# Kernel optimization log

Hardware: AMD Instinct MI355X
Metric: run time of the kernel (lower is better)

The kernel has to match this reference:

```python
import jax, jax.numpy as jnp
import numpy as np

N = 1536          # num nodes
E = 49152         # num edges (avg degree 32)
D_IN = 32         # in_channels_node
D_EA = 2          # in_channels_edge_attr
D_ET = 2          # in_channels_edge_type
EMB = 32          # edge_attr_emb = edge_type_emb = node_emb = out_channels
HEADS = 3
SLOPE = 0.2


def leaky(x):
    return jax.nn.leaky_relu(x, negative_slope=SLOPE)


def setup_inputs() -> dict:
    key = jax.random.key(0)
    ks = jax.random.split(key, 12)
    node_f = jax.random.normal(ks[0], (N, D_IN), dtype=jnp.float32)
    edge_index = jax.random.randint(ks[1], (2, E), 0, N, dtype=jnp.int32)
    edge_attr = jax.random.normal(ks[2], (E, D_EA), dtype=jnp.float32)
    edge_type = jax.random.uniform(ks[3], (E, D_ET), dtype=jnp.float32)
    veh_node_mask = jax.random.bernoulli(ks[4], 0.7, (N,))
    ped_node_mask = jnp.logical_not(veh_node_mask)
    s = 0.1
    W_veh = jax.random.normal(ks[5], (EMB, D_IN), dtype=jnp.float32) * s
    W_ped = jax.random.normal(ks[6], (EMB, D_IN), dtype=jnp.float32) * s
    W_ea = jax.random.normal(ks[7], (EMB, D_EA), dtype=jnp.float32) * s
    W_et = jax.random.normal(ks[8], (EMB, D_ET), dtype=jnp.float32) * s
    # attention_nn: Linear(edge_attr_emb + edge_type_emb + 2*node_emb -> heads)
    W_att = jax.random.normal(ks[9], (HEADS, 2 * EMB + 2 * EMB), dtype=jnp.float32) * s
    # node_update_emb: Linear(edge_attr_emb + node_emb -> out_channels)
    W_upd = jax.random.normal(ks[10], (EMB, 2 * EMB), dtype=jnp.float32) * s
    return dict(node_f=node_f, edge_attr=edge_attr, edge_type=edge_type,
                W_veh=W_veh, W_ped=W_ped, W_ea=W_ea, W_et=W_et,
                W_att=W_att, W_upd=W_upd,
                edge_index=edge_index, veh_node_mask=veh_node_mask,
                ped_node_mask=ped_node_mask)


def reference(node_f, edge_attr, edge_type, W_veh, W_ped, W_ea, W_et,
              W_att, W_upd, edge_index, veh_node_mask, ped_node_mask):
    n = node_f.shape[0]
    src, dst = edge_index[0], edge_index[1]

    # edge embeddings [E, 32] each
    emb_ea = leaky(edge_attr @ W_ea.T)
    emb_et = leaky(edge_type.astype(node_f.dtype) @ W_et.T)
    edge_f = jnp.concatenate([emb_ea, emb_et], axis=-1)        # [E, 64]

    # densify (sparse_coo_tensor -> to_dense sums duplicate indices)
    dense_edge = jnp.zeros((n, n, 2 * EMB), node_f.dtype).at[src, dst].add(edge_f)
    dense_ea = jnp.zeros((n, n, EMB), node_f.dtype).at[src, dst].add(emb_ea)
    adj = jnp.zeros((n, n), node_f.dtype).at[src, dst].add(1.0)

    # type-specific node embedding (ped assignment last, matching torch overwrite order)
    node_emb = jnp.where(veh_node_mask[:, None], node_f @ W_veh.T, 0.0)
    node_emb = jnp.where(ped_node_mask[:, None], node_f @ W_ped.T, node_emb)
    node_emb = leaky(node_emb)                                  # [N, 32]

    # attention scores: split the linear over the concatenated [tar | edge | nbr] features
    W_tar, W_edge, W_nbr = W_att[:, :EMB], W_att[:, EMB:3 * EMB], W_att[:, 3 * EMB:]
    scores = leaky((node_emb @ W_tar.T)[:, None, :]
                   + jnp.einsum('ijc,hc->ijh', dense_edge, W_edge)
                   + (node_emb @ W_nbr.T)[None, :, :])          # [N, N, H]

    scores = jnp.where(adj[:, :, None] == 0.0, jnp.float32(-10000.0), scores)
    attn = jax.nn.softmax(scores, axis=1)                       # softmax over neighbors

    # node update features: Linear over [edge_attr_emb | nbr_emb]; identical across heads
    Wu_e, Wu_n = W_upd[:, :EMB], W_upd[:, EMB:]
    upd = leaky(jnp.einsum('ijc,oc->ijo', dense_ea, Wu_e)
                + (node_emb @ Wu_n.T)[None, :, :])              # [N, N, 32]

    # weighted aggregation over neighbors, then concat heads
    next_node_f = jnp.einsum('ijh,ijo->iho', attn, upd)         # [N, H, 32]
    return next_node_f.reshape(n, HEADS * EMB)
```

## Files before the change

### kernel.cpp

```cpp
#include <hip/hip_runtime.h>
#include <stdint.h>

#define NN 1536
#define EE 49152
#define EMB 32
#define HEADS 3
#define SLOPE 0.2f
#define CAP 72
#define SES 67
#define EBLK (EE/256)
#define NBLK (NN/8)

__device__ __forceinline__ float lrelu(float x){ return x >= 0.f ? x : SLOPE*x; }

__device__ int detect_mask_layout(const unsigned char* p){
  const int* pi = (const int*)p;
  bool ok = true;
  for (int k=0;k<64 && ok;k++){ int v = pi[k]; ok = (v==0 || v==1); }
  if (ok) return 0;
  ok = true;
  for (int k=0;k<256 && ok;k++){ ok = (p[k] <= 1); }
  if (ok) return 1;
  return 2;
}
__device__ bool mask_at(const unsigned char* p, int layout, int i){
  if (layout==0) return ((const int*)p)[i] != 0;
  if (layout==1) return p[i] != 0;
  return ((const float*)p)[i] != 0.f;
}

__global__ __launch_bounds__(256) void k_prep(
    const float* __restrict__ node_f,
    const float* __restrict__ edge_attr, const float* __restrict__ edge_type,
    const float* __restrict__ W_veh, const float* __restrict__ W_ped,
    const float* __restrict__ W_att, const float* __restrict__ W_upd,
    const int* __restrict__ ei, const unsigned char* __restrict__ veh_mask,
    int* __restrict__ cnt, int* __restrict__ bucketD, float4* __restrict__ bucketF,
    float* __restrict__ tar, float* __restrict__ nbr, float* __restrict__ nb)
{
  const int t = threadIdx.x;
  const int b = blockIdx.x;

  if (b < EBLK){
    const int e = b*256 + t;
    const int s = ei[e], d = ei[EE + e];
    const float2 ea = ((const float2*)edge_attr)[e];
    const float2 et = ((const float2*)edge_type)[e];
    const int idx = atomicAdd(&cnt[s], 1);
    if (idx < CAP){
      bucketD[(size_t)s*CAP + idx] = d;
      bucketF[(size_t)s*CAP + idx] = make_float4(ea.x, ea.y, et.x, et.y);
    }
    return;
  }

  __shared__ float sWvehT[EMB*33], sWpedT[EMB*33], sWunT[EMB*33];
  __shared__ float sWt[HEADS*EMB], sWn[HEADS*EMB];
  __shared__ float sF[8*EMB], sEmb[8*EMB];
  __shared__ int layout_s;
  const int i0 = (b - EBLK)*8;
  if (t == 0) layout_s = detect_mask_layout(veh_mask);
  for (int idx=t; idx<EMB*EMB; idx+=256){
    const int mm = idx>>5, kk = idx&31;
    sWvehT[mm*33+kk] = W_veh[idx];
    sWpedT[mm*33+kk] = W_ped[idx];
    sWunT[mm*33+kk]  = W_upd[mm*64 + EMB + kk];
  }
  if (t < HEADS*EMB){
    const int h = t>>5, c = t&31;
    sWt[t] = W_att[h*128 + c];
    sWn[t] = W_att[h*128 + 96 + c];
  }
  sF[t] = node_f[(size_t)i0*EMB + t];
  __syncthreads();

  const int li = t >> 5, m = t & 31;
  const int i = i0 + li;
  const bool veh = mask_at(veh_mask, layout_s, i);
  const float* WT = veh ? sWvehT : sWpedT;
  float a = 0.f;
  #pragma unroll
  for (int k=0;k<EMB;k++) a += sF[li*EMB+k] * WT[m*33+k];
  sEmb[li*EMB+m] = lrelu(a);
  __syncthreads();

  float bb = 0.f;
  #pragma unroll
  for (int k=0;k<EMB;k++) bb += sEmb[li*EMB+k] * sWunT[m*33+k];
  nb[(size_t)i*EMB + m] = bb;
  if (m < 3){
    float v = 0.f;
    #pragma unroll
    for (int k=0;k<EMB;k++) v += sEmb[li*EMB+k] * sWt[m*EMB+k];
    tar[i*4+m] = v;
  } else if (m < 6){
    const int h = m-3;
    float v = 0.f;
    #pragma unroll
    for (int k=0;k<EMB;k++) v += sEmb[li*EMB+k] * sWn[h*EMB+k];
    nbr[i*4+h] = v;
  }
}

__global__ __launch_bounds__(256, 6) void k_rows(
    const int* __restrict__ cnt, const int* __restrict__ bucketD,
    const float4* __restrict__ bucketF,
    const float* __restrict__ W_ea, const float* __restrict__ W_et,
    const float* __restrict__ W_att, const float* __restrict__ W_upd,
    const float* __restrict__ tar, const float* __restrict__ nbr,
    const float* __restrict__ nb, float* __restrict__ out)
{
  const int r = blockIdx.x;
  const int t = threadIdx.x;

  __shared__ int   ld[CAP], canon[CAP], slotidx[CAP], slotof[CAP], cdst[CAP];
  __shared__ float4 pay[CAP];
  __shared__ float sE[CAP*SES];
  __shared__ float sWea[64], sWet[64], sWedge[HEADS*64];
  __shared__ float pp[HEADS*CAP];
  __shared__ float partial[4*96];
  __shared__ float hden[HEADS];
  __shared__ int np_s, hasdup_s;

  if (t < 64){ sWea[t] = W_ea[t]; sWet[t] = W_et[t]; }
  if (t < HEADS*64) sWedge[t] = W_att[(t>>6)*128 + EMB + (t&63)];
  if (t == 0){ np_s = 0; hasdup_s = 0; }

  const int K = min(cnt[r], CAP);

  if (K == 0){
    float* fb = pp;
    if (t < EMB) fb[t] = 0.f;
    __syncthreads();
    for (int idx=t; idx<NN*EMB; idx+=256) atomicAdd(&fb[idx&31], lrelu(nb[idx]));
    __syncthreads();
    if (t < 96) out[(size_t)r*96 + t] = fb[t&31] * (1.0f/NN);
    return;
  }

  for (int i=t; i<K; i+=256){
    const int d = bucketD[(size_t)r*CAP + i];
    ld[i]  = d;
    cdst[i] = d;
    pay[i] = bucketF[(size_t)r*CAP + i];
    canon[i] = i;
  }
  __syncthreads();

  for (int p=t; p<K*K; p+=256){
    const int i = p / K, j = p - i*K;
    if (j < i && ld[i] == ld[j]){ atomicMin(&canon[i], j); hasdup_s = 1; }
  }
  __syncthreads();

  const bool dup = (hasdup_s != 0);
  int Kc = K;
  if (dup){
    for (int i=t; i<K; i+=256){
      if (canon[i] == i){
        const int s2 = atomicAdd(&np_s, 1);
        slotidx[i] = s2;
        cdst[s2]   = ld[i];
      }
    }
    __syncthreads();
    Kc = np_s;
    for (int i=t; i<K; i+=256) slotof[i] = slotidx[canon[i]];
    for (int idx=t; idx<Kc*SES; idx+=256) sE[idx] = 0.f;
    __syncthreads();
  }

  for (int idx=t; idx<K*EMB; idx+=256){
    const int q = idx>>5, m = idx&31;
    const float4 p4 = pay[q];
    const float ea_ = lrelu(p4.x*sWea[2*m] + p4.y*sWea[2*m+1]);
    const float et_ = lrelu(p4.z*sWet[2*m] + p4.w*sWet[2*m+1]);
    if (!dup){
      sE[q*SES + m]      = ea_;
      sE[q*SES + 33 + m] = et_;
    } else {
      const int sl = slotof[q];
      atomicAdd(&sE[sl*SES + m],      ea_);
      atomicAdd(&sE[sl*SES + 33 + m], et_);
    }
  }
  __syncthreads();

  if (t < 192){
    const int h = t >> 6, lane = t & 63;
    const float th = tar[r*4+h];
    float mx = -1e30f;
    for (int q0=0; q0<Kc; q0+=64){
      const int q = q0 + lane;
      if (q < Kc){
        float sev = 0.f;
        #pragma unroll
        for (int k=0;k<EMB;k++)
          sev += sWedge[h*64+k]*sE[q*SES+k] + sWedge[h*64+EMB+k]*sE[q*SES+33+k];
        const float s = lrelu(th + sev + nbr[cdst[q]*4+h]);
        pp[h*CAP+q] = s;
        mx = fmaxf(mx, s);
      }
    }
    #pragma unroll
    for (int d=32; d; d>>=1) mx = fmaxf(mx, __shfl_xor(mx, d, 64));
    float den = 0.f;
    for (int q0=0; q0<Kc; q0+=64){
      const int q = q0 + lane;
      if (q < Kc){
        const float p = __expf(pp[h*CAP+q] - mx);
        pp[h*CAP+q] = p;
        den += p;
      }
    }
    #pragma unroll
    for (int d=32; d; d>>=1) den += __shfl_xor(den, d, 64);
    if (lane == 0) hden[h] = den;
  }
  __syncthreads();

  {
    const int g = t >> 5, o = t & 31;
    const float4* wrow = (const float4*)(W_upd + (size_t)o*64);
    const float4 w0=wrow[0], w1=wrow[1], w2=wrow[2], w3=wrow[3],
                 w4=wrow[4], w5=wrow[5], w6=wrow[6], w7=wrow[7];
    float a0=0.f, a1=0.f, a2=0.f;
    for (int q=g; q<Kc; q+=8){
      const float* se = &sE[q*SES];
      float ev;
      ev  = w0.x*se[0]  + w0.y*se[1]  + w0.z*se[2]  + w0.w*se[3];
      ev += w1.x*se[4]  + w1.y*se[5]  + w1.z*se[6]  + w1.w*se[7];
      ev += w2.x*se[8]  + w2.y*se[9]  + w2.z*se[10] + w2.w*se[11];
      ev += w3.x*se[12] + w3.y*se[13] + w3.z*se[14] + w3.w*se[15];
      ev += w4.x*se[16] + w4.y*se[17] + w4.z*se[18] + w4.w*se[19];
      ev += w5.x*se[20] + w5.y*se[21] + w5.z*se[22] + w5.w*se[23];
      ev += w6.x*se[24] + w6.y*se[25] + w6.z*se[26] + w6.w*se[27];
      ev += w7.x*se[28] + w7.y*se[29] + w7.z*se[30] + w7.w*se[31];
      const float u = lrelu(ev + nb[(size_t)cdst[q]*EMB + o]);
      a0 += pp[0*CAP+q]*u;
      a1 += pp[1*CAP+q]*u;
      a2 += pp[2*CAP+q]*u;
    }
    a0 += __shfl_down(a0, 32, 64);
    a1 += __shfl_down(a1, 32, 64);
    a2 += __shfl_down(a2, 32, 64);
    if ((g & 1) == 0){
      const int gg = g >> 1;
      partial[gg*96 +      o] = a0;
      partial[gg*96 + 32 + o] = a1;
      partial[gg*96 + 64 + o] = a2;
    }
  }
  __syncthreads();
  if (t < 96){
    float s = 0.f;
    #pragma unroll
    for (int g=0; g<4; g++) s += partial[g*96 + t];
    out[(size_t)r*96 + t] = s / hden[t>>5];
  }
}

extern "C" void kernel_launch(void* const* d_in, const int* in_sizes, int n_in,
                              void* d_out, int out_size, void* d_ws, size_t ws_size,
                              hipStream_t stream)
{
  (void)in_sizes; (void)n_in; (void)out_size; (void)ws_size;
  const float* node_f    = (const float*)d_in[0];
  const float* edge_attr = (const float*)d_in[1];
  const float* edge_type = (const float*)d_in[2];
  const float* W_veh     = (const float*)d_in[3];
  const float* W_ped     = (const float*)d_in[4];
  const float* W_ea      = (const float*)d_in[5];
  const float* W_et      = (const float*)d_in[6];
  const float* W_att     = (const float*)d_in[7];
  const float* W_upd     = (const float*)d_in[8];
  const int*   ei        = (const int*)d_in[9];
  const unsigned char* veh_mask = (const unsigned char*)d_in[10];
  float* out = (float*)d_out;

  char* ws = (char*)d_ws;
  const size_t oCnt  = 0;
  const size_t oBktF = oCnt  + (size_t)NN*4;
  const size_t oBktD = oBktF + (size_t)NN*CAP*16;
  const size_t oTar  = oBktD + (size_t)NN*CAP*4;
  const size_t oNbr  = oTar  + (size_t)NN*4*4;
  const size_t oNb   = oNbr  + (size_t)NN*4*4;

  int*    cnt     = (int*)   (ws + oCnt);
  float4* bucketF = (float4*)(ws + oBktF);
  int*    bucketD = (int*)   (ws + oBktD);
  float*  tar     = (float*) (ws + oTar);
  float*  nbr     = (float*) (ws + oNbr);
  float*  nb      = (float*) (ws + oNb);

  hipMemsetAsync(ws + oCnt, 0, (size_t)NN*4, stream);

  k_prep<<<EBLK + NBLK, 256, 0, stream>>>(node_f, edge_attr, edge_type,
                                          W_veh, W_ped, W_att, W_upd,
                                          ei, veh_mask, cnt, bucketD, bucketF,
                                          tar, nbr, nb);
  k_rows<<<NN, 256, 0, stream>>>(cnt, bucketD, bucketF, W_ea, W_et, W_att, W_upd,
                                 tar, nbr, nb, out);
}
```

Measured before the change: 120.3 us.

## Fuse prep and row kernels into one launch with per-block edge scan

Replaces the memset, the bucketing kernel and the per-row kernel with a single kernel where each block handles two source rows. Every block scans the whole edge_index array to collect its rows' edges into shared memory, and recomputes neighbor node embeddings on the fly instead of reading precomputed global buffers. This removes two launches, the memset and the global atomics, at the cost of each block reading all 49K source indices and doing redundant embedding matmuls per neighbor. Correctness relies on __threadfence_block within wavefront groups rather than full barriers.

```diff
diff --git a/kernel.cpp b/kernel.cpp
--- a/kernel.cpp
+++ b/kernel.cpp
@@ -8,8 +8,7 @@
 #define SLOPE 0.2f
 #define CAP 72
 #define SES 67
-#define EBLK (EE/256)
-#define NBLK (NN/8)
+#define GRID (NN/2)
 
 __device__ __forceinline__ float lrelu(float x){ return x >= 0.f ? x : SLOPE*x; }
 
@@ -29,234 +28,277 @@
   return ((const float*)p)[i] != 0.f;
 }
 
-__global__ __launch_bounds__(256) void k_prep(
+__global__ __launch_bounds__(256, 3) void k_all(
     const float* __restrict__ node_f,
     const float* __restrict__ edge_attr, const float* __restrict__ edge_type,
     const float* __restrict__ W_veh, const float* __restrict__ W_ped,
+    const float* __restrict__ W_ea,  const float* __restrict__ W_et,
     const float* __restrict__ W_att, const float* __restrict__ W_upd,
     const int* __restrict__ ei, const unsigned char* __restrict__ veh_mask,
-    int* __restrict__ cnt, int* __restrict__ bucketD, float4* __restrict__ bucketF,
-    float* __restrict__ tar, float* __restrict__ nbr, float* __restrict__ nb)
+    float* __restrict__ out)
 {
   const int t = threadIdx.x;
   const int b = blockIdx.x;
-
-  if (b < EBLK){
-    const int e = b*256 + t;
-    const int s = ei[e], d = ei[EE + e];
-    const float2 ea = ((const float2*)edge_attr)[e];
-    const float2 et = ((const float2*)edge_type)[e];
-    const int idx = atomicAdd(&cnt[s], 1);
-    if (idx < CAP){
-      bucketD[(size_t)s*CAP + idx] = d;
-      bucketF[(size_t)s*CAP + idx] = make_float4(ea.x, ea.y, et.x, et.y);
-    }
-    return;
-  }
+  const int r0 = b*2, r1 = b*2+1;
 
   __shared__ float sWvehT[EMB*33], sWpedT[EMB*33], sWunT[EMB*33];
+  __shared__ float sWea[64], sWet[64], sWedge[HEADS*64];
   __shared__ float sWt[HEADS*EMB], sWn[HEADS*EMB];
-  __shared__ float sF[8*EMB], sEmb[8*EMB];
-  __shared__ int layout_s;
-  const int i0 = (b - EBLK)*8;
-  if (t == 0) layout_s = detect_mask_layout(veh_mask);
+  __shared__ int   le[2][CAP], ldst[2][CAP];
+  __shared__ int   canon[CAP], slotidx[CAP], slotof[CAP], cdst[CAP];
+  __shared__ float4 pay[CAP];
+  __shared__ float sE[CAP*SES];
+  __shared__ float nbL[CAP*33];
+  __shared__ float nbrL[CAP*4];
+  __shared__ float pp[HEADS*CAP];
+  __shared__ float partial[4*96];
+  __shared__ float est[8*33];
+  __shared__ float tarL[2][4];
+  __shared__ float hden[HEADS];
+  __shared__ int kc[2], np_s, hasdup_s, layout_s;
+
   for (int idx=t; idx<EMB*EMB; idx+=256){
     const int mm = idx>>5, kk = idx&31;
     sWvehT[mm*33+kk] = W_veh[idx];
     sWpedT[mm*33+kk] = W_ped[idx];
     sWunT[mm*33+kk]  = W_upd[mm*64 + EMB + kk];
   }
+  if (t < 64){ sWea[t] = W_ea[t]; sWet[t] = W_et[t]; }
+  if (t < HEADS*64) sWedge[t] = W_att[(t>>6)*128 + EMB + (t&63)];
   if (t < HEADS*EMB){
     const int h = t>>5, c = t&31;
     sWt[t] = W_att[h*128 + c];
     sWn[t] = W_att[h*128 + 96 + c];
   }
-  sF[t] = node_f[(size_t)i0*EMB + t];
+  if (t == 0){ layout_s = detect_mask_layout(veh_mask); kc[0] = 0; kc[1] = 0; }
   __syncthreads();
 
-  const int li = t >> 5, m = t & 31;
-  const int i = i0 + li;
-  const bool veh = mask_at(veh_mask, layout_s, i);
-  const float* WT = veh ? sWvehT : sWpedT;
-  float a = 0.f;
-  #pragma unroll
-  for (int k=0;k<EMB;k++) a += sF[li*EMB+k] * WT[m*33+k];
-  sEmb[li*EMB+m] = lrelu(a);
+  {
+    const int4* src4 = (const int4*)ei;
+    for (int i4=t; i4<EE/4; i4+=256){
+      const int4 v = src4[i4];
+      const int e0 = i4*4;
+      #define TRY(comp, eo) do{ const int s_ = (comp); \
+        if (s_ == r0 || s_ == r1){ const int rr_ = (s_ == r1); \
+          const int p_ = atomicAdd(&kc[rr_], 1); \
+          if (p_ < CAP){ le[rr_][p_] = (eo); ldst[rr_][p_] = ei[EE + (eo)]; } } }while(0)
+      TRY(v.x, e0); TRY(v.y, e0+1); TRY(v.z, e0+2); TRY(v.w, e0+3);
+      #undef TRY
+    }
+  }
+  if (t < 64){
+    const int li = t >> 5, m = t & 31;
+    const int i = r0 + li;
+    est[li*33+m] = node_f[(size_t)i*EMB + m];
+    __threadfence_block();
+    const bool veh = mask_at(veh_mask, layout_s, i);
+    const float* WT = veh ? sWvehT : sWpedT;
+    float a = 0.f;
+    #pragma unroll
+    for (int k=0;k<EMB;k++) a += est[li*33+k] * WT[m*33+k];
+    a = lrelu(a);
+    __threadfence_block();
+    est[li*33+m] = a;
+    __threadfence_block();
+    if (m < 3){
+      float v = 0.f;
+      #pragma unroll
+      for (int k=0;k<EMB;k++) v += est[li*33+k] * sWt[m*EMB+k];
+      tarL[li][m] = v;
+    }
+  }
   __syncthreads();
 
-  float bb = 0.f;
-  #pragma unroll
-  for (int k=0;k<EMB;k++) bb += sEmb[li*EMB+k] * sWunT[m*33+k];
-  nb[(size_t)i*EMB + m] = bb;
-  if (m < 3){
-    float v = 0.f;
-    #pragma unroll
-    for (int k=0;k<EMB;k++) v += sEmb[li*EMB+k] * sWt[m*EMB+k];
-    tar[i*4+m] = v;
-  } else if (m < 6){
-    const int h = m-3;
-    float v = 0.f;
-    #pragma unroll
-    for (int k=0;k<EMB;k++) v += sEmb[li*EMB+k] * sWn[h*EMB+k];
-    nbr[i*4+h] = v;
-  }
-}
-
-__global__ __launch_bounds__(256, 6) void k_rows(
-    const int* __restrict__ cnt, const int* __restrict__ bucketD,
-    const float4* __restrict__ bucketF,
-    const float* __restrict__ W_ea, const float* __restrict__ W_et,
-    const float* __restrict__ W_att, const float* __restrict__ W_upd,
-    const float* __restrict__ tar, const float* __restrict__ nbr,
-    const float* __restrict__ nb, float* __restrict__ out)
-{
-  const int r = blockIdx.x;
-  const int t = threadIdx.x;
-
-  __shared__ int   ld[CAP], canon[CAP], slotidx[CAP], slotof[CAP], cdst[CAP];
-  __shared__ float4 pay[CAP];
-  __shared__ float sE[CAP*SES];
-  __shared__ float sWea[64], sWet[64], sWedge[HEADS*64];
-  __shared__ float pp[HEADS*CAP];
-  __shared__ float partial[4*96];
-  __shared__ float hden[HEADS];
-  __shared__ int np_s, hasdup_s;
-
-  if (t < 64){ sWea[t] = W_ea[t]; sWet[t] = W_et[t]; }
-  if (t < HEADS*64) sWedge[t] = W_att[(t>>6)*128 + EMB + (t&63)];
-  if (t == 0){ np_s = 0; hasdup_s = 0; }
-
-  const int K = min(cnt[r], CAP);
-
-  if (K == 0){
-    float* fb = pp;
-    if (t < EMB) fb[t] = 0.f;
-    __syncthreads();
-    for (int idx=t; idx<NN*EMB; idx+=256) atomicAdd(&fb[idx&31], lrelu(nb[idx]));
-    __syncthreads();
-    if (t < 96) out[(size_t)r*96 + t] = fb[t&31] * (1.0f/NN);
-    return;
-  }
-
-  for (int i=t; i<K; i+=256){
-    const int d = bucketD[(size_t)r*CAP + i];
-    ld[i]  = d;
-    cdst[i] = d;
-    pay[i] = bucketF[(size_t)r*CAP + i];
-    canon[i] = i;
-  }
-  __syncthreads();
-
-  for (int p=t; p<K*K; p+=256){
-    const int i = p / K, j = p - i*K;
-    if (j < i && ld[i] == ld[j]){ atomicMin(&canon[i], j); hasdup_s = 1; }
-  }
-  __syncthreads();
-
-  const bool dup = (hasdup_s != 0);
-  int Kc = K;
-  if (dup){
+  for (int rr=0; rr<2; rr++){
+    const int r = r0 + rr;
+    __syncthreads();
+    if (t == 0){ np_s = 0; hasdup_s = 0; }
+
+    const int K = min(kc[rr], CAP);
+
+    if (K == 0){
+      float* fb = pp;
+      if (t < EMB) fb[t] = 0.f;
+      __syncthreads();
+      for (int j=t; j<NN; j+=256){
+        float f[EMB], emb[EMB];
+        #pragma unroll
+        for (int k=0;k<EMB;k++) f[k] = node_f[(size_t)j*EMB + k];
+        const bool veh = mask_at(veh_mask, layout_s, j);
+        const float* WT = veh ? sWvehT : sWpedT;
+        #pragma unroll
+        for (int o=0;o<EMB;o++){
+          float a = 0.f;
+          #pragma unroll
+          for (int k=0;k<EMB;k++) a += WT[o*33+k] * f[k];
+          emb[o] = lrelu(a);
+        }
+        #pragma unroll
+        for (int o=0;o<EMB;o++){
+          float v = 0.f;
+          #pragma unroll
+          for (int k=0;k<EMB;k++) v += sWunT[o*33+k] * emb[k];
+          atomicAdd(&fb[o], lrelu(v));
+        }
+      }
+      __syncthreads();
+      if (t < 96) out[(size_t)r*96 + t] = fb[t&31] * (1.0f/NN);
+      continue;
+    }
+
     for (int i=t; i<K; i+=256){
-      if (canon[i] == i){
-        const int s2 = atomicAdd(&np_s, 1);
-        slotidx[i] = s2;
-        cdst[s2]   = ld[i];
-      }
-    }
-    __syncthreads();
-    Kc = np_s;
-    for (int i=t; i<K; i+=256) slotof[i] = slotidx[canon[i]];
-    for (int idx=t; idx<Kc*SES; idx+=256) sE[idx] = 0.f;
-    __syncthreads();
-  }
-
-  for (int idx=t; idx<K*EMB; idx+=256){
-    const int q = idx>>5, m = idx&31;
-    const float4 p4 = pay[q];
-    const float ea_ = lrelu(p4.x*sWea[2*m] + p4.y*sWea[2*m+1]);
-    const float et_ = lrelu(p4.z*sWet[2*m] + p4.w*sWet[2*m+1]);
-    if (!dup){
-      sE[q*SES + m]      = ea_;
-      sE[q*SES + 33 + m] = et_;
-    } else {
-      const int sl = slotof[q];
-      atomicAdd(&sE[sl*SES + m],      ea_);
-      atomicAdd(&sE[sl*SES + 33 + m], et_);
-    }
-  }
-  __syncthreads();
-
-  if (t < 192){
-    const int h = t >> 6, lane = t & 63;
-    const float th = tar[r*4+h];
-    float mx = -1e30f;
-    for (int q0=0; q0<Kc; q0+=64){
-      const int q = q0 + lane;
-      if (q < Kc){
-        float sev = 0.f;
-        #pragma unroll
-        for (int k=0;k<EMB;k++)
-          sev += sWedge[h*64+k]*sE[q*SES+k] + sWedge[h*64+EMB+k]*sE[q*SES+33+k];
-        const float s = lrelu(th + sev + nbr[cdst[q]*4+h]);
-        pp[h*CAP+q] = s;
-        mx = fmaxf(mx, s);
-      }
-    }
-    #pragma unroll
-    for (int d=32; d; d>>=1) mx = fmaxf(mx, __shfl_xor(mx, d, 64));
-    float den = 0.f;
-    for (int q0=0; q0<Kc; q0+=64){
-      const int q = q0 + lane;
-      if (q < Kc){
-        const float p = __expf(pp[h*CAP+q] - mx);
-        pp[h*CAP+q] = p;
-        den += p;
-      }
-    }
-    #pragma unroll
-    for (int d=32; d; d>>=1) den += __shfl_xor(den, d, 64);
-    if (lane == 0) hden[h] = den;
-  }
-  __syncthreads();
-
-  {
-    const int g = t >> 5, o = t & 31;
-    const float4* wrow = (const float4*)(W_upd + (size_t)o*64);
-    const float4 w0=wrow[0], w1=wrow[1], w2=wrow[2], w3=wrow[3],
-                 w4=wrow[4], w5=wrow[5], w6=wrow[6], w7=wrow[7];
-    float a0=0.f, a1=0.f, a2=0.f;
-    for (int q=g; q<Kc; q+=8){
-      const float* se = &sE[q*SES];
-      float ev;
-      ev  = w0.x*se[0]  + w0.y*se[1]  + w0.z*se[2]  + w0.w*se[3];
-      ev += w1.x*se[4]  + w1.y*se[5]  + w1.z*se[6]  + w1.w*se[7];
-      ev += w2.x*se[8]  + w2.y*se[9]  + w2.z*se[10] + w2.w*se[11];
-      ev += w3.x*se[12] + w3.y*se[13] + w3.z*se[14] + w3.w*se[15];
-      ev += w4.x*se[16] + w4.y*se[17] + w4.z*se[18] + w4.w*se[19];
-      ev += w5.x*se[20] + w5.y*se[21] + w5.z*se[22] + w5.w*se[23];
-      ev += w6.x*se[24] + w6.y*se[25] + w6.z*se[26] + w6.w*se[27];
-      ev += w7.x*se[28] + w7.y*se[29] + w7.z*se[30] + w7.w*se[31];
-      const float u = lrelu(ev + nb[(size_t)cdst[q]*EMB + o]);
-      a0 += pp[0*CAP+q]*u;
-      a1 += pp[1*CAP+q]*u;
-      a2 += pp[2*CAP+q]*u;
-    }
-    a0 += __shfl_down(a0, 32, 64);
-    a1 += __shfl_down(a1, 32, 64);
-    a2 += __shfl_down(a2, 32, 64);
-    if ((g & 1) == 0){
-      const int gg = g >> 1;
-      partial[gg*96 +      o] = a0;
-      partial[gg*96 + 32 + o] = a1;
-      partial[gg*96 + 64 + o] = a2;
-    }
-  }
-  __syncthreads();
-  if (t < 96){
-    float s = 0.f;
-    #pragma unroll
-    for (int g=0; g<4; g++) s += partial[g*96 + t];
-    out[(size_t)r*96 + t] = s / hden[t>>5];
+      const int e = le[rr][i];
+      const float2 ea = ((const float2*)edge_attr)[e];
+      const float2 et = ((const float2*)edge_type)[e];
+      pay[i] = make_float4(ea.x, ea.y, et.x, et.y);
+      cdst[i] = ldst[rr][i];
+      canon[i] = i;
+    }
+    __syncthreads();
+
+    for (int p=t; p<K*K; p+=256){
+      const int i = p / K, j = p - i*K;
+      if (j < i && ldst[rr][i] == ldst[rr][j]){ atomicMin(&canon[i], j); hasdup_s = 1; }
+    }
+    __syncthreads();
+
+    const bool dup = (hasdup_s != 0);
+    int Kc = K;
+    if (dup){
+      for (int i=t; i<K; i+=256){
+        if (canon[i] == i){
+          const int s2 = atomicAdd(&np_s, 1);
+          slotidx[i] = s2;
+          cdst[s2]   = ldst[rr][i];
+        }
+      }
+      __syncthreads();
+      Kc = np_s;
+      for (int i=t; i<K; i+=256) slotof[i] = slotidx[canon[i]];
+      for (int idx=t; idx<Kc*SES; idx+=256) sE[idx] = 0.f;
+      __syncthreads();
+    }
+
+    for (int idx=t; idx<K*EMB; idx+=256){
+      const int q = idx>>5, m = idx&31;
+      const float4 p4 = pay[q];
+      const float ea_ = lrelu(p4.x*sWea[2*m] + p4.y*sWea[2*m+1]);
+      const float et_ = lrelu(p4.z*sWet[2*m] + p4.w*sWet[2*m+1]);
+      if (!dup){
+        sE[q*SES + m]      = ea_;
+        sE[q*SES + 33 + m] = et_;
+      } else {
+        const int sl = slotof[q];
+        atomicAdd(&sE[sl*SES + m],      ea_);
+        atomicAdd(&sE[sl*SES + 33 + m], et_);
+      }
+    }
+
+    {
+      const int g = t >> 5, o = t & 31;
+      float* fst = partial;
+      for (int q0=0; q0<Kc; q0+=8){
+        const int q = q0 + g;
+        if (q < Kc){
+          const int d = cdst[q];
+          fst[g*33+o] = node_f[(size_t)d*EMB + o];
+          __threadfence_block();
+          const bool veh = mask_at(veh_mask, layout_s, d);
+          const float* WT = veh ? sWvehT : sWpedT;
+          float a = 0.f;
+          #pragma unroll
+          for (int k=0;k<EMB;k++) a += fst[g*33+k] * WT[o*33+k];
+          a = lrelu(a);
+          est[g*33+o] = a;
+          __threadfence_block();
+          float nbv = 0.f;
+          #pragma unroll
+          for (int k=0;k<EMB;k++) nbv += est[g*33+k] * sWunT[o*33+k];
+          nbL[q*33+o] = nbv;
+          if (o < 3){
+            float nv = 0.f;
+            #pragma unroll
+            for (int k=0;k<EMB;k++) nv += est[g*33+k] * sWn[o*EMB+k];
+            nbrL[q*4+o] = nv;
+          }
+          __threadfence_block();
+        }
+      }
+    }
+    __syncthreads();
+
+    if (t < 192){
+      const int h = t >> 6, lane = t & 63;
+      const float th = tarL[rr][h];
+      float mx = -1e30f;
+      for (int q0=0; q0<Kc; q0+=64){
+        const int q = q0 + lane;
+        if (q < Kc){
+          float sev = 0.f;
+          #pragma unroll
+          for (int k=0;k<EMB;k++)
+            sev += sWedge[h*64+k]*sE[q*SES+k] + sWedge[h*64+EMB+k]*sE[q*SES+33+k];
+          const float s = lrelu(th + sev + nbrL[q*4+h]);
+          pp[h*CAP+q] = s;
+          mx = fmaxf(mx, s);
+        }
+      }
+      #pragma unroll
+      for (int d=32; d; d>>=1) mx = fmaxf(mx, __shfl_xor(mx, d, 64));
+      float den = 0.f;
+      for (int q0=0; q0<Kc; q0+=64){
+        const int q = q0 + lane;
+        if (q < Kc){
+          const float p = __expf(pp[h*CAP+q] - mx);
+          pp[h*CAP+q] = p;
+          den += p;
+        }
+      }
+      #pragma unroll
+      for (int d=32; d; d>>=1) den += __shfl_xor(den, d, 64);
+      if (lane == 0) hden[h] = den;
+    }
+    __syncthreads();
+
+    {
+      const int g = t >> 5, o = t & 31;
+      const float4* wrow = (const float4*)(W_upd + (size_t)o*64);
+      const float4 w0=wrow[0], w1=wrow[1], w2=wrow[2], w3=wrow[3],
+                   w4=wrow[4], w5=wrow[5], w6=wrow[6], w7=wrow[7];
+      float a0=0.f, a1=0.f, a2=0.f;
+      for (int q=g; q<Kc; q+=8){
+        const float* se = &sE[q*SES];
+        float ev;
+        ev  = w0.x*se[0]  + w0.y*se[1]  + w0.z*se[2]  + w0.w*se[3];
+        ev += w1.x*se[4]  + w1.y*se[5]  + w1.z*se[6]  + w1.w*se[7];
+        ev += w2.x*se[8]  + w2.y*se[9]  + w2.z*se[10] + w2.w*se[11];
+        ev += w3.x*se[12] + w3.y*se[13] + w3.z*se[14] + w3.w*se[15];
+        ev += w4.x*se[16] + w4.y*se[17] + w4.z*se[18] + w4.w*se[19];
+        ev += w5.x*se[20] + w5.y*se[21] + w5.z*se[22] + w5.w*se[23];
+        ev += w6.x*se[24] + w6.y*se[25] + w6.z*se[26] + w6.w*se[27];
+        ev += w7.x*se[28] + w7.y*se[29] + w7.z*se[30] + w7.w*se[31];
+        const float u = lrelu(ev + nbL[q*33+o]);
+        a0 += pp[0*CAP+q]*u;
+        a1 += pp[1*CAP+q]*u;
+        a2 += pp[2*CAP+q]*u;
+      }
+      a0 += __shfl_down(a0, 32, 64);
+      a1 += __shfl_down(a1, 32, 64);
+      a2 += __shfl_down(a2, 32, 64);
+      if ((g & 1) == 0){
+        const int gg = g >> 1;
+        partial[gg*96 +      o] = a0;
+        partial[gg*96 + 32 + o] = a1;
+        partial[gg*96 + 64 + o] = a2;
+      }
+    }
+    __syncthreads();
+    if (t < 96){
+      float s = 0.f;
+      #pragma unroll
+      for (int g=0; g<4; g++) s += partial[g*96 + t];
+      out[(size_t)r*96 + t] = s / hden[t>>5];
+    }
   }
 }
 
@@ -264,7 +306,7 @@
                               void* d_out, int out_size, void* d_ws, size_t ws_size,
                               hipStream_t stream)
 {
-  (void)in_sizes; (void)n_in; (void)out_size; (void)ws_size;
+  (void)in_sizes; (void)n_in; (void)out_size; (void)d_ws; (void)ws_size;
   const float* node_f    = (const float*)d_in[0];
   const float* edge_attr = (const float*)d_in[1];
   const float* edge_type = (const float*)d_in[2];
@@ -278,27 +320,7 @@
   const unsigned char* veh_mask = (const unsigned char*)d_in[10];
   float* out = (float*)d_out;
 
-  char* ws = (char*)d_ws;
-  const size_t oCnt  = 0;
-  const size_t oBktF = oCnt  + (size_t)NN*4;
-  const size_t oBktD = oBktF + (size_t)NN*CAP*16;
-  const size_t oTar  = oBktD + (size_t)NN*CAP*4;
-  const size_t oNbr  = oTar  + (size_t)NN*4*4;
-  const size_t oNb   = oNbr  + (size_t)NN*4*4;
-
-  int*    cnt     = (int*)   (ws + oCnt);
-  float4* bucketF = (float4*)(ws + oBktF);
-  int*    bucketD = (int*)   (ws + oBktD);
-  float*  tar     = (float*) (ws + oTar);
-  float*  nbr     = (float*) (ws + oNbr);
-  float*  nb      = (float*) (ws + oNb);
-
-  hipMemsetAsync(ws + oCnt, 0, (size_t)NN*4, stream);
-
-  k_prep<<<EBLK + NBLK, 256, 0, stream>>>(node_f, edge_attr, edge_type,
-                                          W_veh, W_ped, W_att, W_upd,
-                                          ei, veh_mask, cnt, bucketD, bucketF,
-                                          tar, nbr, nb);
-  k_rows<<<NN, 256, 0, stream>>>(cnt, bucketD, bucketF, W_ea, W_et, W_att, W_upd,
-                                 tar, nbr, nb, out);
+  k_all<<<GRID, 256, 0, stream>>>(node_f, edge_attr, edge_type,
+                                  W_veh, W_ped, W_ea, W_et, W_att, W_upd,
+                                  ei, veh_mask, out);
 }
```

After: 159.4 us. 32.4% more time.
